# Optimization experiments

Measured on AMD Instinct MI355X. Metric: run time of the kernel, lower is better.

Reference implementation:

```python
import jax, jax.numpy as jnp
import numpy as np

NUM_HEADS = 16
THETA = 10000.0


def apply_rope(x, positions, theta=THETA):
    # x: [B, H, S, d_k], positions: [B, S] (broadcast over heads)
    d_k = x.shape[-1]
    inv_freq = theta ** (-jnp.arange(0, d_k // 2, dtype=jnp.float32) * 2.0 / d_k)  # [d_k/2]
    ang = positions[:, None, :, None].astype(jnp.float32) * inv_freq  # [B,1,S,d_k/2]
    cos, sin = jnp.cos(ang), jnp.sin(ang)
    x1 = x[..., 0::2]
    x2 = x[..., 1::2]
    r1 = x1 * cos - x2 * sin
    r2 = x1 * sin + x2 * cos
    # interleave back: [..., d_k/2, 2] -> [..., d_k]
    return jnp.stack([r1, r2], axis=-1).reshape(x.shape)


def setup_inputs() -> dict:
    key = jax.random.key(0)
    ks = jax.random.split(key, 5)
    B, S, D = 1, 4096, 1024
    scale = 1.0 / np.sqrt(D)
    x = jax.random.normal(ks[0], (B, S, D), dtype=jnp.float32)
    Wq = jax.random.normal(ks[1], (D, D), dtype=jnp.float32) * scale
    Wk = jax.random.normal(ks[2], (D, D), dtype=jnp.float32) * scale
    Wv = jax.random.normal(ks[3], (D, D), dtype=jnp.float32) * scale
    Wo = jax.random.normal(ks[4], (D, D), dtype=jnp.float32) * scale
    token_positions = jnp.broadcast_to(jnp.arange(S, dtype=jnp.int32), (B, S))
    return {"x": x, "token_positions": token_positions, "Wq": Wq, "Wk": Wk, "Wv": Wv, "Wo": Wo}


def reference(x, token_positions, Wq, Wk, Wv, Wo):
    B, S, D = x.shape
    H = NUM_HEADS
    d_k = D // H
    # fused QKV projection (Linear: y = x @ W^T, no bias)
    q = jnp.einsum('bsd,ed->bse', x, Wq)
    k = jnp.einsum('bsd,ed->bse', x, Wk)
    v = jnp.einsum('bsd,ed->bse', x, Wv)
    # [B,S,H*dk] -> [B,H,S,dk]
    Q = q.reshape(B, S, H, d_k).transpose(0, 2, 1, 3)
    K = k.reshape(B, S, H, d_k).transpose(0, 2, 1, 3)
    V = v.reshape(B, S, H, d_k).transpose(0, 2, 1, 3)
    Q = apply_rope(Q, token_positions)
    K = apply_rope(K, token_positions)
    scores = jnp.einsum('bhqd,bhkd->bhqk', Q, K) / jnp.sqrt(jnp.float32(d_k))
    causal = jnp.tril(jnp.ones((S, S), dtype=bool))
    scores = jnp.where(causal, scores, -jnp.inf)
    P = jax.nn.softmax(scores, axis=-1)
    out = jnp.einsum('bhqk,bhkd->bhqd', P, V)  # [B,H,S,dk]
    out = out.transpose(0, 2, 1, 3).reshape(B, S, D)
    return jnp.einsum('bsd,ed->bse', out, Wo)
```

## Files before the change

kernel.cpp:

```cpp
#include <hip/hip_runtime.h>
#include <hip/hip_bf16.h>
#include <stdint.h>

#define S_LEN   4096
#define D_MODEL 1024
#define NHEAD   16
#define DK      64

typedef __attribute__((ext_vector_type(8))) __bf16 bf16x8;
typedef __attribute__((ext_vector_type(4))) float  f32x4;
using bf16 = __hip_bfloat16;

#define LOG2E     1.44269504f
#define FREQ_C    0.41524101186092028f

__device__ __forceinline__ void load_lds16(const bf16* g, bf16* l) {
    __builtin_amdgcn_global_load_lds(
        (const __attribute__((address_space(1))) void*)g,
        (__attribute__((address_space(3))) void*)l, 16, 0, 0);
}

__global__ void cvt_all(const float* __restrict__ x,
                        const float* __restrict__ w0, const float* __restrict__ w1,
                        const float* __restrict__ w2, const float* __restrict__ w3,
                        bf16* __restrict__ xb,
                        bf16* __restrict__ b0, bf16* __restrict__ b1,
                        bf16* __restrict__ b2, bf16* __restrict__ b3)
{
    size_t i4 = ((size_t)blockIdx.x * 256 + threadIdx.x) * 4;
    const float* s; bf16* d; size_t off;
    const size_t NX = (size_t)S_LEN * D_MODEL;
    const size_t NW = (size_t)D_MODEL * D_MODEL;
    if (i4 < NX) { s = x; d = xb; off = i4; }
    else {
        size_t j = i4 - NX;
        int sel = (int)(j >> 20);
        off = j & (NW - 1);
        s = sel == 0 ? w0 : sel == 1 ? w1 : sel == 2 ? w2 : w3;
        d = sel == 0 ? b0 : sel == 1 ? b1 : sel == 2 ? b2 : b3;
    }
    float4 v = *(const float4*)&s[off];
    bf16 t[4] __attribute__((aligned(8)));
    t[0] = __float2bfloat16(v.x); t[1] = __float2bfloat16(v.y);
    t[2] = __float2bfloat16(v.z); t[3] = __float2bfloat16(v.w);
    *(uint64_t*)&d[off] = *(const uint64_t*)t;
}

__global__ __launch_bounds__(256) void qkv_gemm(
    const bf16* __restrict__ Xb,
    const bf16* __restrict__ Wq, const bf16* __restrict__ Wk, const bf16* __restrict__ Wv,
    const int* __restrict__ pos,
    bf16* __restrict__ Qb, bf16* __restrict__ Kb, bf16* __restrict__ VtG)
{
    const int K = D_MODEL, N = D_MODEL;
    int z = blockIdx.z;
    const bf16* B = (z == 0) ? Wq : (z == 1) ? Wk : Wv;

    __shared__ __align__(16) bf16 As[2][128 * 32];
    __shared__ __align__(16) bf16 Bs[2][128 * 32];
    __shared__ __align__(16) bf16 Ts[4][64 * 24];

    int row0 = blockIdx.y * 128;
    int col0 = blockIdx.x * 128;
    int tid  = threadIdx.x;
    int wv   = tid >> 6, lane = tid & 63;
    int m16  = lane & 15, quad = lane >> 4;
    int wr   = (wv >> 1) * 64, wc = (wv & 1) * 64;
    int l4   = lane >> 2, l3 = (lane & 3) * 8;

    const bf16* ga_base = Xb + (size_t)(row0 + wv * 16 + l4) * K + l3;
    const bf16* gb_base = B  + (size_t)(col0 + wv * 16 + l4) * K + l3;

    auto stage = [&](int k0, int buf) {
        load_lds16(ga_base + k0,            &As[buf][wv * 512]);
        load_lds16(ga_base + k0 + 64 * K,   &As[buf][2048 + wv * 512]);
        load_lds16(gb_base + k0,            &Bs[buf][wv * 512]);
        load_lds16(gb_base + k0 + 64 * K,   &Bs[buf][2048 + wv * 512]);
    };

    f32x4 acc[4][4];
    #pragma unroll
    for (int i = 0; i < 4; i++)
        #pragma unroll
        for (int j = 0; j < 4; j++) acc[i][j] = (f32x4){0.f, 0.f, 0.f, 0.f};

    stage(0, 0);
    for (int k0 = 0; k0 < K; k0 += 32) {
        __syncthreads();
        int buf = (k0 >> 5) & 1;
        if (k0 + 32 < K) stage(k0 + 32, buf ^ 1);
        bf16x8 a[4], b[4];
        #pragma unroll
        for (int mi = 0; mi < 4; mi++) a[mi] = *(const bf16x8*)&As[buf][(wr + mi * 16 + m16) * 32 + quad * 8];
        #pragma unroll
        for (int ni = 0; ni < 4; ni++) b[ni] = *(const bf16x8*)&Bs[buf][(wc + ni * 16 + m16) * 32 + quad * 8];
        #pragma unroll
        for (int mi = 0; mi < 4; mi++)
            #pragma unroll
            for (int ni = 0; ni < 4; ni++)
                acc[mi][ni] = __builtin_amdgcn_mfma_f32_16x16x32_bf16(a[mi], b[ni], acc[mi][ni], 0, 0, 0);
    }

    if (z < 2) {
        bf16* O = (z == 0) ? Qb : Kb;
        const float qscale = (z == 0) ? 0.125f * LOG2E : 1.0f;
        const bool odd = (m16 & 1);
        float invf[4];
        #pragma unroll
        for (int ni = 0; ni < 4; ni++) {
            int hd = (wc + ni * 16 + m16) & 63;
            invf[ni] = exp2f(-(float)(hd >> 1) * FREQ_C);
        }
        #pragma unroll
        for (int mi = 0; mi < 4; mi++) {
            #pragma unroll
            for (int r = 0; r < 4; r++) {
                int gr = row0 + wr + mi * 16 + quad * 4 + r;
                float p = (float)pos[gr];
                #pragma unroll
                for (int ni = 0; ni < 4; ni++) {
                    float own = acc[mi][ni][r];
                    float other = __shfl_xor(own, 1);
                    float sn, cs;
                    __sincosf(p * invf[ni], &sn, &cs);
                    float rot = odd ? (other * sn + own * cs) : (own * cs - other * sn);
                    int gc = col0 + wc + ni * 16 + m16;
                    O[(size_t)gr * N + gc] = __float2bfloat16(rot * qscale);
                }
            }
        }
    } else {
        #pragma unroll
        for (int mi = 0; mi < 4; mi++) {
            #pragma unroll
            for (int nt = 0; nt < 4; nt++) {
                bf16 t4[4] __attribute__((aligned(8)));
                #pragma unroll
                for (int r = 0; r < 4; r++) t4[r] = __float2bfloat16(acc[mi][nt][r]);
                *(uint64_t*)&Ts[wv][(nt * 16 + m16) * 24 + quad * 4] = *(const uint64_t*)t4;
            }
            #pragma unroll
            for (int rep = 0; rep < 2; rep++) {
                int c  = (lane >> 1) + rep * 32;
                int r8 = lane & 1;
                bf16x8 val = *(const bf16x8*)&Ts[wv][c * 24 + r8 * 8];
                int gc = col0 + wc + c;
                int gr = row0 + wr + mi * 16 + r8 * 8;
                *(bf16x8*)&VtG[(size_t)gc * S_LEN + gr] = val;
            }
        }
    }
}

__global__ __launch_bounds__(256) void out_gemm(
    const bf16* __restrict__ A_, const bf16* __restrict__ B,
    float* __restrict__ C)
{
    const int K = D_MODEL, N = D_MODEL;
    __shared__ __align__(16) bf16 As[2][64 * 32];
    __shared__ __align__(16) bf16 Bs[2][128 * 32];

    int row0 = blockIdx.y * 64;
    int col0 = blockIdx.x * 128;
    int tid  = threadIdx.x;
    int wv   = tid >> 6, lane = tid & 63;
    int m16  = lane & 15, quad = lane >> 4;
    int wr   = (wv >> 1) * 32, wc = (wv & 1) * 64;
    int l4   = lane >> 2, l3 = (lane & 3) * 8;

    const bf16* ga_base = A_ + (size_t)(row0 + wv * 16 + l4) * K + l3;
    const bf16* gb_base = B  + (size_t)(col0 + wv * 16 + l4) * K + l3;

    auto stage = [&](int k0, int buf) {
        load_lds16(ga_base + k0,            &As[buf][wv * 512]);
        load_lds16(gb_base + k0,            &Bs[buf][wv * 512]);
        load_lds16(gb_base + k0 + 64 * K,   &Bs[buf][2048 + wv * 512]);
    };

    f32x4 acc[2][4];
    #pragma unroll
    for (int i = 0; i < 2; i++)
        #pragma unroll
        for (int j = 0; j < 4; j++) acc[i][j] = (f32x4){0.f, 0.f, 0.f, 0.f};

    stage(0, 0);
    for (int k0 = 0; k0 < K; k0 += 32) {
        __syncthreads();
        int buf = (k0 >> 5) & 1;
        if (k0 + 32 < K) stage(k0 + 32, buf ^ 1);
        bf16x8 a[2], b[4];
        #pragma unroll
        for (int mi = 0; mi < 2; mi++) a[mi] = *(const bf16x8*)&As[buf][(wr + mi * 16 + m16) * 32 + quad * 8];
        #pragma unroll
        for (int ni = 0; ni < 4; ni++) b[ni] = *(const bf16x8*)&Bs[buf][(wc + ni * 16 + m16) * 32 + quad * 8];
        #pragma unroll
        for (int mi = 0; mi < 2; mi++)
            #pragma unroll
            for (int ni = 0; ni < 4; ni++)
                acc[mi][ni] = __builtin_amdgcn_mfma_f32_16x16x32_bf16(a[mi], b[ni], acc[mi][ni], 0, 0, 0);
    }

    #pragma unroll
    for (int mi = 0; mi < 2; mi++)
        #pragma unroll
        for (int ni = 0; ni < 4; ni++)
            #pragma unroll
            for (int r = 0; r < 4; r++) {
                int gr = row0 + wr + mi * 16 + quad * 4 + r;
                int gc = col0 + wc + ni * 16 + m16;
                C[(size_t)gr * N + gc] = acc[mi][ni][r];
            }
}

__global__ __launch_bounds__(256) void attn_kernel(
    const bf16* __restrict__ Qb, const bf16* __restrict__ Kb, const bf16* __restrict__ VtG,
    bf16* __restrict__ Attn)
{
    int bx  = blockIdx.x;
    int h   = bx & 15;
    int qt  = 63 - (bx >> 4);
    int tid = threadIdx.x;
    int wv  = tid >> 6, lane = tid & 63;
    int m16 = lane & 15, quad = lane >> 4;
    int l4  = lane >> 2, l3 = (lane & 3) * 8;
    int q0  = qt * 64;
    int hc  = h * DK;

    __shared__ __align__(16) bf16 KT[2][64 * 32];
    __shared__ __align__(16) bf16 VT[2][64 * 32];
    __shared__ __align__(16) bf16 Ps[64 * 72];

    const bf16* kg = Kb  + (size_t)(wv * 16 + l4) * D_MODEL + hc + l3;
    const bf16* vg = VtG + (size_t)(hc + wv * 16 + l4) * S_LEN + l3;

    auto stage = [&](int kb) {
        size_t ko = (size_t)kb * 64;
        load_lds16(kg + ko * D_MODEL,        &KT[0][wv * 512]);
        load_lds16(kg + ko * D_MODEL + 32,   &KT[1][wv * 512]);
        load_lds16(vg + ko,                  &VT[0][wv * 512]);
        load_lds16(vg + ko + 32,             &VT[1][wv * 512]);
    };

    const int qrow = q0 + wv * 16 + m16;
    bf16x8 aq0 = *(const bf16x8*)&Qb[(size_t)qrow * D_MODEL + hc + quad * 8];
    bf16x8 aq1 = *(const bf16x8*)&Qb[(size_t)qrow * D_MODEL + hc + 32 + quad * 8];

    float l_part[4];
    f32x4 o[4];
    #pragma unroll
    for (int r = 0; r < 4; r++) { l_part[r] = 0.f; o[r] = (f32x4){0.f, 0.f, 0.f, 0.f}; }

    const float SHIFT2 = 8.0f * LOG2E;

    for (int kb = 0; kb <= qt; ++kb) {
        __syncthreads();
        stage(kb);
        __syncthreads();
        int kbase = kb * 64;

        f32x4 sAcc[4];
        #pragma unroll
        for (int nt = 0; nt < 4; nt++) {
            bf16x8 b0 = *(const bf16x8*)&KT[0][(nt * 16 + m16) * 32 + quad * 8];
            bf16x8 b1 = *(const bf16x8*)&KT[1][(nt * 16 + m16) * 32 + quad * 8];
            f32x4 zv = (f32x4){0.f, 0.f, 0.f, 0.f};
            zv = __builtin_amdgcn_mfma_f32_16x16x32_bf16(aq0, b0, zv, 0, 0, 0);
            zv = __builtin_amdgcn_mfma_f32_16x16x32_bf16(aq1, b1, zv, 0, 0, 0);
            sAcc[nt] = zv;
        }

        if (kb == qt) {
            #pragma unroll
            for (int nt = 0; nt < 4; nt++) {
                int colg = kbase + nt * 16 + m16;
                #pragma unroll
                for (int r = 0; r < 4; r++) {
                    int rowg = q0 + wv * 16 + quad * 4 + r;
                    if (colg > rowg) sAcc[nt][r] = -1e30f;
                }
            }
        }

        #pragma unroll
        for (int nt = 0; nt < 4; nt++) {
            #pragma unroll
            for (int r = 0; r < 4; r++) {
                float pv = exp2f(sAcc[nt][r] - SHIFT2);
                sAcc[nt][r] = pv;
                l_part[r] += pv;
            }
        }

        #pragma unroll
        for (int nt = 0; nt < 4; nt++)
            #pragma unroll
            for (int r = 0; r < 4; r++)
                Ps[(wv * 16 + quad * 4 + r) * 72 + nt * 16 + m16] = __float2bfloat16(sAcc[nt][r]);

        bf16x8 ap0 = *(const bf16x8*)&Ps[(wv * 16 + m16) * 72 + quad * 8];
        bf16x8 ap1 = *(const bf16x8*)&Ps[(wv * 16 + m16) * 72 + 32 + quad * 8];

        #pragma unroll
        for (int nt = 0; nt < 4; nt++) {
            bf16x8 v0 = *(const bf16x8*)&VT[0][(nt * 16 + m16) * 32 + quad * 8];
            bf16x8 v1 = *(const bf16x8*)&VT[1][(nt * 16 + m16) * 32 + quad * 8];
            o[nt] = __builtin_amdgcn_mfma_f32_16x16x32_bf16(ap0, v0, o[nt], 0, 0, 0);
            o[nt] = __builtin_amdgcn_mfma_f32_16x16x32_bf16(ap1, v1, o[nt], 0, 0, 0);
        }
    }

    float inv[4];
    #pragma unroll
    for (int r = 0; r < 4; r++) {
        float l = l_part[r];
        l += __shfl_xor(l, 1); l += __shfl_xor(l, 2);
        l += __shfl_xor(l, 4); l += __shfl_xor(l, 8);
        inv[r] = 1.0f / l;
    }
    #pragma unroll
    for (int nt = 0; nt < 4; nt++)
        #pragma unroll
        for (int r = 0; r < 4; r++) {
            int rowg = q0 + wv * 16 + quad * 4 + r;
            Attn[(size_t)rowg * D_MODEL + hc + nt * 16 + m16] = __float2bfloat16(o[nt][r] * inv[r]);
        }
}

extern "C" void kernel_launch(void* const* d_in, const int* in_sizes, int n_in,
                              void* d_out, int out_size, void* d_ws, size_t ws_size,
                              hipStream_t stream)
{
    const float* x  = (const float*)d_in[0];
    const int*   pos= (const int*)d_in[1];
    const float* Wq = (const float*)d_in[2];
    const float* Wk = (const float*)d_in[3];
    const float* Wv = (const float*)d_in[4];
    const float* Wo = (const float*)d_in[5];
    float* out = (float*)d_out;

    char* ws = (char*)d_ws;
    bf16*  xb   = (bf16*) (ws);
    bf16*  wqb  = (bf16*) (ws + ( 8ull << 20));
    bf16*  wkb  = (bf16*) (ws + (10ull << 20));
    bf16*  wvb  = (bf16*) (ws + (12ull << 20));
    bf16*  wob  = (bf16*) (ws + (14ull << 20));
    bf16*  Qb   = (bf16*) (ws + (16ull << 20));
    bf16*  Kb   = (bf16*) (ws + (24ull << 20));
    bf16*  VtG  = (bf16*) (ws + (32ull << 20));
    bf16*  Attn = (bf16*) (ws + (40ull << 20));

    cvt_all<<<8192, 256, 0, stream>>>(x, Wq, Wk, Wv, Wo, xb, wqb, wkb, wvb, wob);

    qkv_gemm<<<dim3(8, 32, 3), 256, 0, stream>>>(xb, wqb, wkb, wvb, pos, Qb, Kb, VtG);

    attn_kernel<<<dim3(1024), 256, 0, stream>>>(Qb, Kb, VtG, Attn);

    out_gemm<<<dim3(8, 64), 256, 0, stream>>>(Attn, wob, out);
}
```

Before: 227.2 us.

## Keep attention probabilities in registers via transposed QK^T and MFMA row sums

Computes the score tile transposed (K as the A operand, Q as B) so each lane's exponentiated probabilities can feed the PV MFMA directly as the B operand. This removes the per-block LDS round trip through the Ps buffer. The inputs are zero-padded to half of the 32-wide K dimension, so the PV step issues twice as many MFMAs. Row sums come from an MFMA against a ones vector instead of shuffle reductions, and the constant softmax shift is dropped in favour of the raw exp2 builtin. The output is staged through LDS so the global stores are wide and coalesced.

```diff
diff --git a/kernel.cpp b/kernel.cpp
--- a/kernel.cpp
+++ b/kernel.cpp
@@ -226,104 +226,117 @@
     int q0  = qt * 64;
     int hc  = h * DK;
 
-    __shared__ __align__(16) bf16 KT[2][64 * 32];
-    __shared__ __align__(16) bf16 VT[2][64 * 32];
-    __shared__ __align__(16) bf16 Ps[64 * 72];
+    __shared__ __align__(16) bf16 smem[8192];
+    bf16* KT0 = smem;
+    bf16* KT1 = smem + 2048;
+    bf16* VT0 = smem + 4096;
+    bf16* VT1 = smem + 6144;
 
     const bf16* kg = Kb  + (size_t)(wv * 16 + l4) * D_MODEL + hc + l3;
     const bf16* vg = VtG + (size_t)(hc + wv * 16 + l4) * S_LEN + l3;
 
     auto stage = [&](int kb) {
         size_t ko = (size_t)kb * 64;
-        load_lds16(kg + ko * D_MODEL,        &KT[0][wv * 512]);
-        load_lds16(kg + ko * D_MODEL + 32,   &KT[1][wv * 512]);
-        load_lds16(vg + ko,                  &VT[0][wv * 512]);
-        load_lds16(vg + ko + 32,             &VT[1][wv * 512]);
+        load_lds16(kg + ko * D_MODEL,        KT0 + wv * 512);
+        load_lds16(kg + ko * D_MODEL + 32,   KT1 + wv * 512);
+        load_lds16(vg + ko,                  VT0 + wv * 512);
+        load_lds16(vg + ko + 32,             VT1 + wv * 512);
     };
 
     const int qrow = q0 + wv * 16 + m16;
     bf16x8 aq0 = *(const bf16x8*)&Qb[(size_t)qrow * D_MODEL + hc + quad * 8];
     bf16x8 aq1 = *(const bf16x8*)&Qb[(size_t)qrow * D_MODEL + hc + 32 + quad * 8];
 
-    float l_part[4];
+    const bf16 one_b = __float2bfloat16(1.0f);
+    const bf16 zero_b = __float2bfloat16(0.0f);
+    bf16x8 onesF;
+    {
+        bf16 t[8] __attribute__((aligned(16)));
+        #pragma unroll
+        for (int j = 0; j < 8; j++) t[j] = (j < 4) ? one_b : zero_b;
+        onesF = *(const bf16x8*)t;
+    }
+
     f32x4 o[4];
-    #pragma unroll
-    for (int r = 0; r < 4; r++) { l_part[r] = 0.f; o[r] = (f32x4){0.f, 0.f, 0.f, 0.f}; }
-
-    const float SHIFT2 = 8.0f * LOG2E;
+    f32x4 lacc;
+    #pragma unroll
+    for (int t = 0; t < 4; t++) o[t] = (f32x4){0.f, 0.f, 0.f, 0.f};
+    lacc = (f32x4){0.f, 0.f, 0.f, 0.f};
+
+    const int q_g = q0 + wv * 16 + m16;
 
     for (int kb = 0; kb <= qt; ++kb) {
         __syncthreads();
         stage(kb);
         __syncthreads();
-        int kbase = kb * 64;
-
-        f32x4 sAcc[4];
+
+        f32x4 sT[4];
         #pragma unroll
         for (int nt = 0; nt < 4; nt++) {
-            bf16x8 b0 = *(const bf16x8*)&KT[0][(nt * 16 + m16) * 32 + quad * 8];
-            bf16x8 b1 = *(const bf16x8*)&KT[1][(nt * 16 + m16) * 32 + quad * 8];
+            bf16x8 ka = *(const bf16x8*)&KT0[(nt * 16 + m16) * 32 + quad * 8];
+            bf16x8 kb_ = *(const bf16x8*)&KT1[(nt * 16 + m16) * 32 + quad * 8];
             f32x4 zv = (f32x4){0.f, 0.f, 0.f, 0.f};
-            zv = __builtin_amdgcn_mfma_f32_16x16x32_bf16(aq0, b0, zv, 0, 0, 0);
-            zv = __builtin_amdgcn_mfma_f32_16x16x32_bf16(aq1, b1, zv, 0, 0, 0);
-            sAcc[nt] = zv;
+            zv = __builtin_amdgcn_mfma_f32_16x16x32_bf16(ka, aq0, zv, 0, 0, 0);
+            zv = __builtin_amdgcn_mfma_f32_16x16x32_bf16(kb_, aq1, zv, 0, 0, 0);
+            sT[nt] = zv;
         }
 
         if (kb == qt) {
+            int keyb = kb * 64 + quad * 4;
+            #pragma unroll
+            for (int nt = 0; nt < 4; nt++)
+                #pragma unroll
+                for (int r = 0; r < 4; r++)
+                    if (keyb + nt * 16 + r > q_g) sT[nt][r] = -1e30f;
+        }
+
+        bf16x8 pf[4];
+        #pragma unroll
+        for (int nt = 0; nt < 4; nt++) {
+            bf16 t[8] __attribute__((aligned(16)));
+            #pragma unroll
+            for (int r = 0; r < 4; r++) t[r] = __float2bfloat16(__builtin_amdgcn_exp2f(sT[nt][r]));
+            #pragma unroll
+            for (int r = 4; r < 8; r++) t[r] = zero_b;
+            pf[nt] = *(const bf16x8*)t;
+        }
+
+        #pragma unroll
+        for (int nt = 0; nt < 4; nt++)
+            lacc = __builtin_amdgcn_mfma_f32_16x16x32_bf16(onesF, pf[nt], lacc, 0, 0, 0);
+
+        #pragma unroll
+        for (int mt = 0; mt < 4; mt++) {
             #pragma unroll
             for (int nt = 0; nt < 4; nt++) {
-                int colg = kbase + nt * 16 + m16;
-                #pragma unroll
-                for (int r = 0; r < 4; r++) {
-                    int rowg = q0 + wv * 16 + quad * 4 + r;
-                    if (colg > rowg) sAcc[nt][r] = -1e30f;
-                }
-            }
-        }
-
-        #pragma unroll
-        for (int nt = 0; nt < 4; nt++) {
-            #pragma unroll
-            for (int r = 0; r < 4; r++) {
-                float pv = exp2f(sAcc[nt][r] - SHIFT2);
-                sAcc[nt][r] = pv;
-                l_part[r] += pv;
-            }
-        }
-
-        #pragma unroll
-        for (int nt = 0; nt < 4; nt++)
-            #pragma unroll
-            for (int r = 0; r < 4; r++)
-                Ps[(wv * 16 + quad * 4 + r) * 72 + nt * 16 + m16] = __float2bfloat16(sAcc[nt][r]);
-
-        bf16x8 ap0 = *(const bf16x8*)&Ps[(wv * 16 + m16) * 72 + quad * 8];
-        bf16x8 ap1 = *(const bf16x8*)&Ps[(wv * 16 + m16) * 72 + 32 + quad * 8];
-
-        #pragma unroll
-        for (int nt = 0; nt < 4; nt++) {
-            bf16x8 v0 = *(const bf16x8*)&VT[0][(nt * 16 + m16) * 32 + quad * 8];
-            bf16x8 v1 = *(const bf16x8*)&VT[1][(nt * 16 + m16) * 32 + quad * 8];
-            o[nt] = __builtin_amdgcn_mfma_f32_16x16x32_bf16(ap0, v0, o[nt], 0, 0, 0);
-            o[nt] = __builtin_amdgcn_mfma_f32_16x16x32_bf16(ap1, v1, o[nt], 0, 0, 0);
-        }
-    }
-
-    float inv[4];
-    #pragma unroll
-    for (int r = 0; r < 4; r++) {
-        float l = l_part[r];
-        l += __shfl_xor(l, 1); l += __shfl_xor(l, 2);
-        l += __shfl_xor(l, 4); l += __shfl_xor(l, 8);
-        inv[r] = 1.0f / l;
-    }
-    #pragma unroll
-    for (int nt = 0; nt < 4; nt++)
-        #pragma unroll
-        for (int r = 0; r < 4; r++) {
-            int rowg = q0 + wv * 16 + quad * 4 + r;
-            Attn[(size_t)rowg * D_MODEL + hc + nt * 16 + m16] = __float2bfloat16(o[nt][r] * inv[r]);
-        }
+                const bf16* vsrc = (nt < 2) ? VT0 : VT1;
+                bf16 va[8] __attribute__((aligned(16)));
+                *(uint64_t*)va = *(const uint64_t*)&vsrc[(mt * 16 + m16) * 32 + (nt & 1) * 16 + quad * 4];
+                *(uint64_t*)(va + 4) = 0;
+                o[mt] = __builtin_amdgcn_mfma_f32_16x16x32_bf16(*(const bf16x8*)va, pf[nt], o[mt], 0, 0, 0);
+            }
+        }
+    }
+
+    __syncthreads();
+
+    float inv = 1.0f / lacc[0];
+    bf16* Ls = smem + wv * 1152;
+    #pragma unroll
+    for (int mt = 0; mt < 4; mt++) {
+        bf16 t[4] __attribute__((aligned(8)));
+        #pragma unroll
+        for (int r = 0; r < 4; r++) t[r] = __float2bfloat16(o[mt][r] * inv);
+        *(uint64_t*)&Ls[m16 * 72 + mt * 16 + quad * 4] = *(const uint64_t*)t;
+    }
+    {
+        int q_ = lane >> 2, c_ = lane & 3;
+        bf16x8 v0 = *(const bf16x8*)&Ls[q_ * 72 + c_ * 8];
+        bf16x8 v1 = *(const bf16x8*)&Ls[q_ * 72 + 32 + c_ * 8];
+        size_t rowg = (size_t)(q0 + wv * 16 + q_) * D_MODEL + hc;
+        *(bf16x8*)&Attn[rowg + c_ * 8]      = v0;
+        *(bf16x8*)&Attn[rowg + 32 + c_ * 8] = v1;
+    }
 }
 
 extern "C" void kernel_launch(void* const* d_in, const int* in_sizes, int n_in,
```

New measurement: 295.5 us. +30.1%, slower.
